# Kernel optimization log

Hardware: AMD Instinct MI355X
Metric: run time of the kernel (lower is better)

## Reference

```python
import jax, jax.numpy as jnp
import numpy as np

B, H, W = 2, 56, 56
D_MODEL, D_STATE, D_CONV, DT_RANK, K = 96, 16, 3, 6, 4
D_INNER = 192  # expand=2.0 * d_model


def _hscan1(x):
    # torch get_horizontal_scan1: flip odd columns along H; involution. x: (B,C,H,W)
    cols = (jnp.arange(x.shape[3]) % 2) == 1
    return jnp.where(cols[None, None, None, :], x[:, :, ::-1, :], x)


def _vscan1(x):
    # torch get_vertical_scan1: flip odd rows along W, then transpose H<->W. (B,C,H,W)->(B,C,W,H)
    rows = (jnp.arange(x.shape[2]) % 2) == 1
    x = jnp.where(rows[None, None, :, None], x[:, :, :, ::-1], x)
    return jnp.swapaxes(x, 2, 3)


def _revert_vscan1(x):
    # inverse of _vscan1. x: (B,C,W,H) -> (B,C,H,W)
    x = jnp.swapaxes(x, 2, 3)
    rows = (jnp.arange(x.shape[2]) % 2) == 1
    return jnp.where(rows[None, None, :, None], x[:, :, :, ::-1], x)


def _selective_scan(u, delta, A, Bs, Cs, D, delta_bias):
    # u, delta: (B, K*d, L); A: (K*d, N); Bs, Cs: (B, K, N, L); D: (K*d,)
    Bb, KD, L = u.shape
    k = Bs.shape[1]
    d = KD // k
    N = A.shape[1]
    delta = jax.nn.softplus(delta + delta_bias[None, :, None])
    u4 = u.reshape(Bb, k, d, L)
    dt4 = delta.reshape(Bb, k, d, L)
    A4 = A.reshape(k, d, N)
    dA = jnp.exp(jnp.einsum('bkdl,kdn->lbkdn', dt4, A4))           # (L,B,K,d,N)
    dBu = jnp.einsum('bkdl,bknl,bkdl->lbkdn', dt4, Bs, u4)          # (L,B,K,d,N)
    Ct = jnp.transpose(Cs, (3, 0, 1, 2))                            # (L,B,K,N)
    h0 = jnp.zeros((Bb, k, d, N), u.dtype)

    def step(h, inp):
        dA_t, dBu_t, C_t = inp
        h = dA_t * h + dBu_t
        y = jnp.einsum('bkdn,bkn->bkd', h, C_t)
        return h, y

    _, ys = jax.lax.scan(step, h0, (dA, dBu, Ct))                   # ys: (L,B,K,d)
    y = jnp.transpose(ys, (1, 2, 3, 0)).reshape(Bb, KD, L)
    return y + u * D[None, :, None]


def reference(x, in_proj_w, conv_w, conv_b, x_proj_weight, dt_projs_weight,
              dt_projs_bias, A_logs, Ds, out_norm_w, out_norm_b, out_proj_w):
    Bb, Hh, Ww, _ = x.shape
    L = Hh * Ww
    xz = jnp.einsum('bhwc,ec->bhwe', x, in_proj_w)
    xc, z = jnp.split(xz, 2, axis=-1)
    xc = jnp.transpose(xc, (0, 3, 1, 2))                            # (B, d_inner, H, W)
    xc = jax.lax.conv_general_dilated(xc, conv_w, (1, 1), ((1, 1), (1, 1)),
                                      feature_group_count=D_INNER)
    xc = jax.nn.silu(xc + conv_b[None, :, None, None])
    # torch code mutates x in place: vertical scan sees the h-scanned tensor
    x1 = _hscan1(xc)
    x_hw = x1.reshape(Bb, 1, D_INNER, L)
    x2 = _vscan1(x1)
    x_wh = x2.reshape(Bb, 1, D_INNER, L)
    xs = jnp.concatenate([x_hw, x_wh, x_hw[..., ::-1], x_wh[..., ::-1]], axis=1)  # (B,K,d,L)
    x_dbl = jnp.einsum('bkdl,kcd->bkcl', xs, x_proj_weight)
    dts, Bs, Cs = jnp.split(x_dbl, [DT_RANK, DT_RANK + D_STATE], axis=2)
    dts = jnp.einsum('bkrl,kdr->bkdl', dts, dt_projs_weight)
    u = xs.reshape(Bb, K * D_INNER, L)
    delta = dts.reshape(Bb, K * D_INNER, L)
    A = -jnp.exp(A_logs)
    out_y = _selective_scan(u, delta, A, Bs, Cs, Ds, dt_projs_bias.reshape(-1))
    oy = out_y.reshape(Bb, K, D_INNER, L)
    # revert scans back to a common spatial layout and sum
    s0 = _hscan1(oy[:, 0].reshape(Bb, D_INNER, Hh, Ww))
    s2 = _hscan1(oy[:, 2, :, ::-1].reshape(Bb, D_INNER, Hh, Ww))
    s1 = _hscan1(_revert_vscan1(oy[:, 1].reshape(Bb, D_INNER, Ww, Hh)))
    s3 = _hscan1(_revert_vscan1(oy[:, 3, :, ::-1].reshape(Bb, D_INNER, Ww, Hh)))
    y = (s0 + s1 + s2 + s3).reshape(Bb, D_INNER, L)
    y = jnp.transpose(y, (0, 2, 1))                                 # (B, L, d_inner)
    mu = jnp.mean(y, axis=-1, keepdims=True)
    var = jnp.var(y, axis=-1, keepdims=True)
    y = (y - mu) / jnp.sqrt(var + 1e-5) * out_norm_w + out_norm_b
    y = y.reshape(Bb, Hh, Ww, D_INNER) * jax.nn.silu(z)
    return jnp.einsum('bhwd,cd->bhwc', y, out_proj_w)


def setup_inputs():
    key = jax.random.key(0)
    ks = jax.random.split(key, 8)
    s = 0.02
    return {
        "x": jax.random.normal(ks[0], (B, H, W, D_MODEL), jnp.float32),
        "in_proj_w": jax.random.normal(ks[1], (2 * D_INNER, D_MODEL), jnp.float32) * s,
        "conv_w": jax.random.normal(ks[2], (D_INNER, 1, D_CONV, D_CONV), jnp.float32) * s,
        "conv_b": jnp.zeros((D_INNER,), jnp.float32),
        "x_proj_weight": jax.random.normal(ks[3], (K, DT_RANK + 2 * D_STATE, D_INNER), jnp.float32) * s,
        "dt_projs_weight": jax.random.normal(ks[4], (K, D_INNER, DT_RANK), jnp.float32) * (DT_RANK ** -0.5),
        "dt_projs_bias": jax.random.uniform(ks[5], (K, D_INNER), jnp.float32, -4.6, -2.3),
        "A_logs": jnp.log(jnp.tile(jnp.arange(1, D_STATE + 1, dtype=jnp.float32)[None, :], (K * D_INNER, 1))),
        "Ds": jnp.ones((K * D_INNER,), jnp.float32),
        "out_norm_w": jnp.ones((D_INNER,), jnp.float32),
        "out_norm_b": jnp.zeros((D_INNER,), jnp.float32),
        "out_proj_w": jax.random.normal(ks[6], (D_MODEL, D_INNER), jnp.float32) * s,
    }
```

## Files before the change

kernel.cpp:

```cpp
#include <hip/hip_runtime.h>
#include <hip/hip_bf16.h>

#define BB 2
#define HH 56
#define WW 56
#define LL (HH*WW)
#define DM 96
#define DI 192
#define NS 16
#define DTR 6
#define KK 4
#define CDBL (DTR + 2*NS)
#define CS 32
#define NC 98
#define ROWS (BB*KK*DI)

#define IP_BM 32
__global__ __launch_bounds__(256) void k_inproj(const float* __restrict__ x,
                                                const float* __restrict__ w,
                                                float* __restrict__ xcpre,
                                                float* __restrict__ zsilu) {
    __shared__ float xl[IP_BM*100];
    __shared__ float wl[64*100];
    int t = threadIdx.x;
    int bl0 = blockIdx.x * IP_BM;
    for (int idx = t; idx < IP_BM*96; idx += 256) {
        int r = idx/96, c = idx%96;
        xl[r*100+c] = x[(bl0+r)*DM + c];
    }
    int pg = t >> 4, eg = t & 15;
    for (int nc = 0; nc < 6; ++nc) {
        __syncthreads();
        for (int idx = t; idx < 64*96; idx += 256) {
            int r = idx/96, c = idx%96;
            wl[r*100+c] = w[(nc*64+r)*DM + c];
        }
        __syncthreads();
        float acc[2][4] = {};
        #pragma unroll 4
        for (int k = 0; k < 96; ++k) {
            float a0 = xl[(pg*2+0)*100+k];
            float a1 = xl[(pg*2+1)*100+k];
            float b0 = wl[(eg*4+0)*100+k];
            float b1 = wl[(eg*4+1)*100+k];
            float b2 = wl[(eg*4+2)*100+k];
            float b3 = wl[(eg*4+3)*100+k];
            acc[0][0] = fmaf(a0,b0,acc[0][0]); acc[0][1] = fmaf(a0,b1,acc[0][1]);
            acc[0][2] = fmaf(a0,b2,acc[0][2]); acc[0][3] = fmaf(a0,b3,acc[0][3]);
            acc[1][0] = fmaf(a1,b0,acc[1][0]); acc[1][1] = fmaf(a1,b1,acc[1][1]);
            acc[1][2] = fmaf(a1,b2,acc[1][2]); acc[1][3] = fmaf(a1,b3,acc[1][3]);
        }
        #pragma unroll
        for (int j = 0; j < 2; ++j) {
            int bl = bl0 + pg*2 + j;
            #pragma unroll
            for (int jj = 0; jj < 4; ++jj) {
                int e = nc*64 + eg*4 + jj;
                float v = acc[j][jj];
                if (e < DI) xcpre[(size_t)bl*DI + e] = v;
                else        zsilu[(size_t)bl*DI + (e-DI)] = v / (1.f + expf(-v));
            }
        }
    }
}

__global__ __launch_bounds__(DI) void k_conv(const float* __restrict__ xcpre,
                                             const float* __restrict__ cw,
                                             const float* __restrict__ cb,
                                             float* __restrict__ xs0,
                                             float* __restrict__ xs1) {
    int bl = blockIdx.x;
    int b = bl / LL, l = bl % LL;
    int h = l / WW, w = l % WW;
    int c = threadIdx.x;
    float acc = cb[c];
    #pragma unroll
    for (int dh = -1; dh <= 1; ++dh) {
        int hh = h + dh;
        if (hh < 0 || hh >= HH) continue;
        #pragma unroll
        for (int dw = -1; dw <= 1; ++dw) {
            int ww2 = w + dw;
            if (ww2 < 0 || ww2 >= WW) continue;
            acc = fmaf(xcpre[(b*LL + hh*WW + ww2)*DI + c],
                       cw[c*9 + (dh+1)*3 + (dw+1)], acc);
        }
    }
    float v = acc / (1.f + expf(-acc));
    int i  = (w & 1) ? (HH-1-h) : h;
    int l0 = i*WW + w;
    int l1 = ((i & 1) ? (WW-1-w) : w)*HH + i;
    xs0[(b*LL + l0)*DI + c] = v;
    xs1[(b*LL + l1)*DI + c] = v;
}

#define TL 32
__global__ __launch_bounds__(256) void k_proj(const float* __restrict__ xs0,
                                              const float* __restrict__ xs1,
                                              const float* __restrict__ xpw,
                                              const float* __restrict__ dtw,
                                              const float* __restrict__ dtb,
                                              float* __restrict__ delta,
                                              float* __restrict__ Bsb,
                                              float* __restrict__ Csb) {
    int tile = blockIdx.x, k = blockIdx.y, b = blockIdx.z;
    int t = threadIdx.x;
    __shared__ float Wl[CDBL*DI];
    __shared__ float dtWl[DI*DTR];
    __shared__ float dtbl[DI];
    __shared__ float Xl[TL*193];
    __shared__ float dblL[DTR*33];

    for (int idx = t; idx < CDBL*DI; idx += 256) Wl[idx] = xpw[k*CDBL*DI + idx];
    for (int idx = t; idx < DI*DTR;  idx += 256) dtWl[idx] = dtw[k*DI*DTR + idx];
    if (t < DI) dtbl[t] = dtb[k*DI + t];
    const float* src = (k & 1) ? xs1 : xs0;
    for (int idx = t; idx < TL*DI; idx += 256) {
        int ll = idx / DI, i = idx % DI;
        int lg = tile*TL + ll;
        int lp = (k >= 2) ? (LL-1-lg) : lg;
        Xl[ll*193 + i] = src[(b*LL + lp)*DI + i];
    }
    __syncthreads();

    for (int idx = t; idx < CDBL*TL; idx += 256) {
        int c = idx >> 5, ll = idx & 31;
        float acc = 0.f;
        #pragma unroll 8
        for (int i = 0; i < DI; ++i) acc = fmaf(Wl[c*DI + i], Xl[ll*193 + i], acc);
        int lg = tile*TL + ll;
        if (c < DTR) {
            dblL[c*33 + ll] = acc;
        } else if (c < DTR + NS) {
            Bsb[((b*KK + k)*LL + lg)*NS + (c - DTR)] = acc;
        } else {
            Csb[((b*KK + k)*LL + lg)*NS + (c - DTR - NS)] = acc;
        }
    }
    __syncthreads();

    for (int idx = t; idx < DI*TL; idx += 256) {
        int d = idx % DI, ll = idx / DI;
        float acc = dtbl[d];
        #pragma unroll
        for (int r = 0; r < DTR; ++r) acc = fmaf(dtWl[d*DTR + r], dblL[r*33 + ll], acc);
        float sp = fmaxf(acc, 0.f) + log1pf(expf(-fabsf(acc)));
        delta[((b*KK + k)*LL + tile*TL + ll)*DI + d] = sp;
    }
}

__global__ __launch_bounds__(192) void k_scan1(const float* __restrict__ delta,
                                               const float* __restrict__ xs0,
                                               const float* __restrict__ xs1,
                                               const float* __restrict__ Bsb,
                                               const float* __restrict__ A_logs,
                                               float* __restrict__ P,
                                               float* __restrict__ Hend) {
    int c = blockIdx.x, bk = blockIdx.y;
    int k = bk & 3, b = bk >> 2;
    int d = threadIdx.x;
    int kd = k*DI + d;
    __shared__ float Bl[CS*NS];
    const float* bsrc = Bsb + ((size_t)bk*LL + c*CS)*NS;
    for (int i = threadIdx.x; i < CS*NS/4; i += 192)
        ((float4*)Bl)[i] = ((const float4*)bsrc)[i];

    float A[NS], h[NS], p[NS];
    #pragma unroll
    for (int q = 0; q < 4; ++q) {
        float4 av = *(const float4*)&A_logs[kd*NS + 4*q];
        A[4*q+0] = -expf(av.x); A[4*q+1] = -expf(av.y);
        A[4*q+2] = -expf(av.z); A[4*q+3] = -expf(av.w);
    }
    #pragma unroll
    for (int n = 0; n < NS; ++n) { h[n] = 0.f; p[n] = 1.f; }
    __syncthreads();

    const bool rev = (k >= 2);
    const float* dp = delta + ((size_t)bk*LL + c*CS)*DI + d;
    const float* up = ((k & 1) ? xs1 : xs0) + (size_t)b*LL*DI + d;
    const int l0 = c*CS;

    #pragma unroll 2
    for (int i = 0; i < CS; ++i) {
        float dt = dp[(size_t)i*DI];
        int lp = rev ? (LL-1-(l0+i)) : (l0+i);
        float u = up[(size_t)lp*DI];
        float dtu = dt * u;
        float Bv[NS];
        #pragma unroll
        for (int q = 0; q < 4; ++q)
            *(float4*)&Bv[4*q] = *(const float4*)&Bl[i*NS + 4*q];
        #pragma unroll
        for (int n = 0; n < NS; ++n) {
            float dA = __expf(dt * A[n]);
            h[n] = fmaf(dA, h[n], dtu * Bv[n]);
            p[n] *= dA;
        }
    }
    size_t obase = ((size_t)c*ROWS + bk*DI + d)*NS;
    #pragma unroll
    for (int q = 0; q < 4; ++q) {
        *(float4*)&P[obase + 4*q]    = make_float4(p[4*q], p[4*q+1], p[4*q+2], p[4*q+3]);
        *(float4*)&Hend[obase + 4*q] = make_float4(h[4*q], h[4*q+1], h[4*q+2], h[4*q+3]);
    }
}

__global__ __launch_bounds__(256) void k_scanmid(const float* __restrict__ P,
                                                 const float* __restrict__ Hend,
                                                 float* __restrict__ Hin) {
    int tid = blockIdx.x*256 + threadIdx.x;
    float h = 0.f;
    for (int c = 0; c < NC; ++c) {
        size_t idx = (size_t)c*(ROWS*NS) + tid;
        Hin[idx] = h;
        h = fmaf(P[idx], h, Hend[idx]);
    }
}

__global__ __launch_bounds__(192) void k_scan2(const float* __restrict__ delta,
                                               const float* __restrict__ xs0,
                                               const float* __restrict__ xs1,
                                               const float* __restrict__ Bsb,
                                               const float* __restrict__ Csb,
                                               const float* __restrict__ A_logs,
                                               const float* __restrict__ Ds,
                                               const float* __restrict__ Hin,
                                               float* __restrict__ oy) {
    int c = blockIdx.x, bk = blockIdx.y;
    int k = bk & 3, b = bk >> 2;
    int d = threadIdx.x;
    int kd = k*DI + d;
    __shared__ float Bl[CS*NS];
    __shared__ float Cl[CS*NS];
    const float* bsrc = Bsb + ((size_t)bk*LL + c*CS)*NS;
    const float* csrc = Csb + ((size_t)bk*LL + c*CS)*NS;
    for (int i = threadIdx.x; i < CS*NS/4; i += 192) {
        ((float4*)Bl)[i] = ((const float4*)bsrc)[i];
        ((float4*)Cl)[i] = ((const float4*)csrc)[i];
    }

    float A[NS], h[NS];
    #pragma unroll
    for (int q = 0; q < 4; ++q) {
        float4 av = *(const float4*)&A_logs[kd*NS + 4*q];
        A[4*q+0] = -expf(av.x); A[4*q+1] = -expf(av.y);
        A[4*q+2] = -expf(av.z); A[4*q+3] = -expf(av.w);
    }
    size_t ibase = ((size_t)c*ROWS + bk*DI + d)*NS;
    #pragma unroll
    for (int q = 0; q < 4; ++q) {
        float4 hv = *(const float4*)&Hin[ibase + 4*q];
        h[4*q+0] = hv.x; h[4*q+1] = hv.y; h[4*q+2] = hv.z; h[4*q+3] = hv.w;
    }
    const float Dv = Ds[kd];
    __syncthreads();

    const bool rev = (k >= 2);
    const float* dp = delta + ((size_t)bk*LL + c*CS)*DI + d;
    const float* up = ((k & 1) ? xs1 : xs0) + (size_t)b*LL*DI + d;
    float* yp = oy + ((size_t)bk*LL + c*CS)*DI + d;
    const int l0 = c*CS;

    #pragma unroll 2
    for (int i = 0; i < CS; ++i) {
        float dt = dp[(size_t)i*DI];
        int lp = rev ? (LL-1-(l0+i)) : (l0+i);
        float u = up[(size_t)lp*DI];
        float dtu = dt * u;
        float Bv[NS], Cv[NS];
        #pragma unroll
        for (int q = 0; q < 4; ++q) {
            *(float4*)&Bv[4*q] = *(const float4*)&Bl[i*NS + 4*q];
            *(float4*)&Cv[4*q] = *(const float4*)&Cl[i*NS + 4*q];
        }
        float acc = 0.f;
        #pragma unroll
        for (int n = 0; n < NS; ++n) {
            float dA = __expf(dt * A[n]);
            h[n] = fmaf(dA, h[n], dtu * Bv[n]);
            acc = fmaf(h[n], Cv[n], acc);
        }
        yp[(size_t)i*DI] = fmaf(u, Dv, acc);
    }
}

#define OP_BM 32
__global__ __launch_bounds__(256) void k_out(const float* __restrict__ oy,
                                             const float* __restrict__ zsilu,
                                             const float* __restrict__ onw,
                                             const float* __restrict__ onb,
                                             const float* __restrict__ opw,
                                             float* __restrict__ out) {
    __shared__ float yv[OP_BM*196];
    __shared__ float wl[96*68];
    int t = threadIdx.x;
    int bl0 = blockIdx.x * OP_BM;
    int lane = t & 63, wv = t >> 6;

    for (int pp = 0; pp < 8; ++pp) {
        int p = wv*8 + pp;
        int bl = bl0 + p;
        int b = bl / LL, l = bl % LL;
        int h = l / WW, w2 = l % WW;
        int i = (w2 & 1) ? (HH-1-h) : h;
        int l0 = i*WW + w2;
        int l1 = ((i & 1) ? (WW-1-w2) : w2)*HH + i;
        size_t base = (size_t)b*KK*LL*DI;
        float yd[3]; float s1 = 0.f, s2 = 0.f;
        #pragma unroll
        for (int j = 0; j < 3; ++j) {
            int c = lane + j*64;
            float v = oy[base + (size_t)(0*LL + l0)*DI + c]
                    + oy[base + (size_t)(1*LL + l1)*DI + c]
                    + oy[base + (size_t)(2*LL + (LL-1-l0))*DI + c]
                    + oy[base + (size_t)(3*LL + (LL-1-l1))*DI + c];
            yd[j] = v; s1 += v; s2 += v*v;
        }
        #pragma unroll
        for (int m = 1; m < 64; m <<= 1) { s1 += __shfl_xor(s1, m); s2 += __shfl_xor(s2, m); }
        float mu  = s1 / DI;
        float var = s2 / DI - mu*mu;
        float ry  = rsqrtf(var + 1e-5f);
        #pragma unroll
        for (int j = 0; j < 3; ++j) {
            int c = lane + j*64;
            float yn = (yd[j] - mu) * ry * onw[c] + onb[c];
            yv[p*196 + c] = yn * zsilu[(size_t)bl*DI + c];
        }
    }

    int pg = t >> 5, eg = t & 31;
    float acc[4][3] = {};
    for (int kc = 0; kc < 3; ++kc) {
        __syncthreads();
        for (int idx = t; idx < 96*64; idx += 256) {
            int r = idx >> 6, c = idx & 63;
            wl[r*68 + c] = opw[r*DI + kc*64 + c];
        }
        __syncthreads();
        #pragma unroll 4
        for (int kk = 0; kk < 64; ++kk) {
            float a[4], bq[3];
            #pragma unroll
            for (int j = 0; j < 4; ++j)  a[j]  = yv[(pg*4+j)*196 + kc*64 + kk];
            #pragma unroll
            for (int jj = 0; jj < 3; ++jj) bq[jj] = wl[(eg*3+jj)*68 + kk];
            #pragma unroll
            for (int j = 0; j < 4; ++j)
                #pragma unroll
                for (int jj = 0; jj < 3; ++jj)
                    acc[j][jj] = fmaf(a[j], bq[jj], acc[j][jj]);
        }
    }
    #pragma unroll
    for (int j = 0; j < 4; ++j) {
        int bl = bl0 + pg*4 + j;
        #pragma unroll
        for (int jj = 0; jj < 3; ++jj)
            out[(size_t)bl*DM + eg*3 + jj] = acc[j][jj];
    }
}

extern "C" void kernel_launch(void* const* d_in, const int* in_sizes, int n_in,
                              void* d_out, int out_size, void* d_ws, size_t ws_size,
                              hipStream_t stream) {
    const float* x      = (const float*)d_in[0];
    const float* ipw    = (const float*)d_in[1];
    const float* convw  = (const float*)d_in[2];
    const float* convb  = (const float*)d_in[3];
    const float* xpw    = (const float*)d_in[4];
    const float* dtw    = (const float*)d_in[5];
    const float* dtb    = (const float*)d_in[6];
    const float* A_logs = (const float*)d_in[7];
    const float* Ds     = (const float*)d_in[8];
    const float* onw    = (const float*)d_in[9];
    const float* onb    = (const float*)d_in[10];
    const float* opw    = (const float*)d_in[11];
    float* out = (float*)d_out;

    float* ws = (float*)d_ws;
    const size_t SZ_BLD  = (size_t)BB*LL*DI;
    const size_t SZ_BKLD = (size_t)BB*KK*LL*DI;
    const size_t SZ_BKLN = (size_t)BB*KK*LL*NS;
    const size_t SZ_ST   = (size_t)NC*ROWS*NS;
    float* xcpre = ws;
    float* zsilu = xcpre + SZ_BLD;
    float* xs0   = zsilu + SZ_BLD;
    float* xs1   = xs0   + SZ_BLD;
    float* delta = xs1   + SZ_BLD;
    float* Bsb   = delta + SZ_BKLD;
    float* Csb   = Bsb   + SZ_BKLN;
    float* oy    = Csb   + SZ_BKLN;
    float* Hin   = oy    + SZ_BKLD;
    float* Hend  = oy;
    float* P     = oy + SZ_ST;

    k_inproj<<<(BB*LL)/IP_BM, 256, 0, stream>>>(x, ipw, xcpre, zsilu);
    k_conv<<<BB*LL, DI, 0, stream>>>(xcpre, convw, convb, xs0, xs1);
    dim3 g3(LL/TL, KK, BB);
    k_proj<<<g3, 256, 0, stream>>>(xs0, xs1, xpw, dtw, dtb, delta, Bsb, Csb);
    dim3 gs(NC, BB*KK);
    k_scan1<<<gs, 192, 0, stream>>>(delta, xs0, xs1, Bsb, A_logs, P, Hend);
    k_scanmid<<<(ROWS*NS)/256, 256, 0, stream>>>(P, Hend, Hin);
    k_scan2<<<gs, 192, 0, stream>>>(delta, xs0, xs1, Bsb, Csb, A_logs, Ds, Hin, oy);
    k_out<<<(BB*LL)/OP_BM, 256, 0, stream>>>(oy, zsilu, onw, onb, opw, out);
}
```

Before: 273.7 us.

## Register-block x_proj GEMM in k_proj with K-chunked shared tiles

Rewrites k_proj so the x_proj matmul streams K in 48-wide chunks through small shared tiles with float4 loads. Each thread computes a 3x4 register block of outputs over a 64-position tile. The tile was 32 positions and one dot product per thread. dt_proj weights and biases now sit in registers, exploiting that each thread's channel index is fixed across iterations. The aim is less shared memory, higher occupancy and more FMA reuse per load, at the cost of extra syncs and half as many blocks.

```diff
diff --git a/kernel.cpp b/kernel.cpp
--- a/kernel.cpp
+++ b/kernel.cpp
@@ -94,7 +94,11 @@
     xs1[(b*LL + l1)*DI + c] = v;
 }
 
-#define TL 32
+#define TL 64
+#define KCH 48
+#define NKC 4
+#define XSTR 52
+#define WSTR 52
 __global__ __launch_bounds__(256) void k_proj(const float* __restrict__ xs0,
                                               const float* __restrict__ xs1,
                                               const float* __restrict__ xpw,
@@ -104,48 +108,118 @@
                                               float* __restrict__ Bsb,
                                               float* __restrict__ Csb) {
     int tile = blockIdx.x, k = blockIdx.y, b = blockIdx.z;
+    int bk = b*KK + k;
     int t = threadIdx.x;
-    __shared__ float Wl[CDBL*DI];
-    __shared__ float dtWl[DI*DTR];
-    __shared__ float dtbl[DI];
-    __shared__ float Xl[TL*193];
-    __shared__ float dblL[DTR*33];
-
-    for (int idx = t; idx < CDBL*DI; idx += 256) Wl[idx] = xpw[k*CDBL*DI + idx];
-    for (int idx = t; idx < DI*DTR;  idx += 256) dtWl[idx] = dtw[k*DI*DTR + idx];
-    if (t < DI) dtbl[t] = dtb[k*DI + t];
+    __shared__ float Xl[TL*XSTR];
+    __shared__ float Wl[39*WSTR];
+    __shared__ float dblL[DTR*68];
+
     const float* src = (k & 1) ? xs1 : xs0;
-    for (int idx = t; idx < TL*DI; idx += 256) {
-        int ll = idx / DI, i = idx % DI;
-        int lg = tile*TL + ll;
-        int lp = (k >= 2) ? (LL-1-lg) : lg;
-        Xl[ll*193 + i] = src[(b*LL + lp)*DI + i];
+    const bool rev = (k >= 2);
+    int cp = t >> 4, lp = t & 15;
+
+    float acc[3][4] = {};
+    for (int kc = 0; kc < NKC; ++kc) {
+        __syncthreads();
+        for (int idx = t; idx < 39*12; idx += 256) {
+            int r = idx/12, q = idx%12;
+            float4 v = (r < CDBL)
+                ? ((const float4*)(xpw + (size_t)k*CDBL*DI + (size_t)r*DI + kc*KCH))[q]
+                : make_float4(0.f,0.f,0.f,0.f);
+            *(float4*)&Wl[r*WSTR + 4*q] = v;
+        }
+        for (int idx = t; idx < TL*12; idx += 256) {
+            int ll = idx/12, q = idx%12;
+            int lg = tile*TL + ll;
+            int lpos = rev ? (LL-1-lg) : lg;
+            *(float4*)&Xl[ll*XSTR + 4*q] =
+                ((const float4*)(src + (size_t)(b*LL + lpos)*DI + kc*KCH))[q];
+        }
+        __syncthreads();
+        if (cp < 13) {
+            const float4* w0 = (const float4*)&Wl[(3*cp+0)*WSTR];
+            const float4* w1 = (const float4*)&Wl[(3*cp+1)*WSTR];
+            const float4* w2 = (const float4*)&Wl[(3*cp+2)*WSTR];
+            const float4* x0 = (const float4*)&Xl[(lp    )*XSTR];
+            const float4* x1 = (const float4*)&Xl[(lp+16)*XSTR];
+            const float4* x2 = (const float4*)&Xl[(lp+32)*XSTR];
+            const float4* x3 = (const float4*)&Xl[(lp+48)*XSTR];
+            #pragma unroll
+            for (int q = 0; q < 12; ++q) {
+                float4 wa = w0[q], wb = w1[q], wc = w2[q];
+                float4 xa = x0[q], xb = x1[q], xc = x2[q], xd = x3[q];
+                acc[0][0]=fmaf(wa.x,xa.x,acc[0][0]); acc[0][0]=fmaf(wa.y,xa.y,acc[0][0]);
+                acc[0][0]=fmaf(wa.z,xa.z,acc[0][0]); acc[0][0]=fmaf(wa.w,xa.w,acc[0][0]);
+                acc[0][1]=fmaf(wa.x,xb.x,acc[0][1]); acc[0][1]=fmaf(wa.y,xb.y,acc[0][1]);
+                acc[0][1]=fmaf(wa.z,xb.z,acc[0][1]); acc[0][1]=fmaf(wa.w,xb.w,acc[0][1]);
+                acc[0][2]=fmaf(wa.x,xc.x,acc[0][2]); acc[0][2]=fmaf(wa.y,xc.y,acc[0][2]);
+                acc[0][2]=fmaf(wa.z,xc.z,acc[0][2]); acc[0][2]=fmaf(wa.w,xc.w,acc[0][2]);
+                acc[0][3]=fmaf(wa.x,xd.x,acc[0][3]); acc[0][3]=fmaf(wa.y,xd.y,acc[0][3]);
+                acc[0][3]=fmaf(wa.z,xd.z,acc[0][3]); acc[0][3]=fmaf(wa.w,xd.w,acc[0][3]);
+                acc[1][0]=fmaf(wb.x,xa.x,acc[1][0]); acc[1][0]=fmaf(wb.y,xa.y,acc[1][0]);
+                acc[1][0]=fmaf(wb.z,xa.z,acc[1][0]); acc[1][0]=fmaf(wb.w,xa.w,acc[1][0]);
+                acc[1][1]=fmaf(wb.x,xb.x,acc[1][1]); acc[1][1]=fmaf(wb.y,xb.y,acc[1][1]);
+                acc[1][1]=fmaf(wb.z,xb.z,acc[1][1]); acc[1][1]=fmaf(wb.w,xb.w,acc[1][1]);
+                acc[1][2]=fmaf(wb.x,xc.x,acc[1][2]); acc[1][2]=fmaf(wb.y,xc.y,acc[1][2]);
+                acc[1][2]=fmaf(wb.z,xc.z,acc[1][2]); acc[1][2]=fmaf(wb.w,xc.w,acc[1][2]);
+                acc[1][3]=fmaf(wb.x,xd.x,acc[1][3]); acc[1][3]=fmaf(wb.y,xd.y,acc[1][3]);
+                acc[1][3]=fmaf(wb.z,xd.z,acc[1][3]); acc[1][3]=fmaf(wb.w,xd.w,acc[1][3]);
+                acc[2][0]=fmaf(wc.x,xa.x,acc[2][0]); acc[2][0]=fmaf(wc.y,xa.y,acc[2][0]);
+                acc[2][0]=fmaf(wc.z,xa.z,acc[2][0]); acc[2][0]=fmaf(wc.w,xa.w,acc[2][0]);
+                acc[2][1]=fmaf(wc.x,xb.x,acc[2][1]); acc[2][1]=fmaf(wc.y,xb.y,acc[2][1]);
+                acc[2][1]=fmaf(wc.z,xb.z,acc[2][1]); acc[2][1]=fmaf(wc.w,xb.w,acc[2][1]);
+                acc[2][2]=fmaf(wc.x,xc.x,acc[2][2]); acc[2][2]=fmaf(wc.y,xc.y,acc[2][2]);
+                acc[2][2]=fmaf(wc.z,xc.z,acc[2][2]); acc[2][2]=fmaf(wc.w,xc.w,acc[2][2]);
+                acc[2][3]=fmaf(wc.x,xd.x,acc[2][3]); acc[2][3]=fmaf(wc.y,xd.y,acc[2][3]);
+                acc[2][3]=fmaf(wc.z,xd.z,acc[2][3]); acc[2][3]=fmaf(wc.w,xd.w,acc[2][3]);
+            }
+        }
+    }
+    if (cp < 13) {
+        #pragma unroll
+        for (int ci = 0; ci < 3; ++ci) {
+            int c = 3*cp + ci;
+            if (c < CDBL) {
+                #pragma unroll
+                for (int li = 0; li < 4; ++li) {
+                    int ll = lp + 16*li;
+                    int lg = tile*TL + ll;
+                    float v = acc[ci][li];
+                    if (c < DTR)          dblL[c*68 + ll] = v;
+                    else if (c < DTR+NS)  Bsb[((size_t)bk*LL + lg)*NS + (c-DTR)] = v;
+                    else                  Csb[((size_t)bk*LL + lg)*NS + (c-DTR-NS)] = v;
+                }
+            }
+        }
     }
     __syncthreads();
 
-    for (int idx = t; idx < CDBL*TL; idx += 256) {
-        int c = idx >> 5, ll = idx & 31;
-        float acc = 0.f;
-        #pragma unroll 8
-        for (int i = 0; i < DI; ++i) acc = fmaf(Wl[c*DI + i], Xl[ll*193 + i], acc);
-        int lg = tile*TL + ll;
-        if (c < DTR) {
-            dblL[c*33 + ll] = acc;
-        } else if (c < DTR + NS) {
-            Bsb[((b*KK + k)*LL + lg)*NS + (c - DTR)] = acc;
-        } else {
-            Csb[((b*KK + k)*LL + lg)*NS + (c - DTR - NS)] = acc;
-        }
-    }
-    __syncthreads();
-
-    for (int idx = t; idx < DI*TL; idx += 256) {
-        int d = idx % DI, ll = idx / DI;
-        float acc = dtbl[d];
-        #pragma unroll
-        for (int r = 0; r < DTR; ++r) acc = fmaf(dtWl[d*DTR + r], dblL[r*33 + ll], acc);
-        float sp = fmaxf(acc, 0.f) + log1pf(expf(-fabsf(acc)));
-        delta[((b*KK + k)*LL + tile*TL + ll)*DI + d] = sp;
+    float wr0[DTR], wr1[DTR], wr2[DTR], bb0, bb1, bb2;
+    {
+        int d0 = t % DI, d1 = (t+64) % DI, d2 = (t+128) % DI;
+        #pragma unroll
+        for (int r = 0; r < DTR; ++r) {
+            wr0[r] = dtw[((size_t)k*DI + d0)*DTR + r];
+            wr1[r] = dtw[((size_t)k*DI + d1)*DTR + r];
+            wr2[r] = dtw[((size_t)k*DI + d2)*DTR + r];
+        }
+        bb0 = dtb[k*DI + d0]; bb1 = dtb[k*DI + d1]; bb2 = dtb[k*DI + d2];
+    }
+    float* dbase = delta + ((size_t)bk*LL + (size_t)tile*TL)*DI;
+    for (int j3 = 0; j3 < 16; ++j3) {
+        #pragma unroll
+        for (int jj = 0; jj < 3; ++jj) {
+            int j = j3*3 + jj;
+            int idx = t + 256*j;
+            int d = idx % DI;
+            int ll = idx / DI;
+            float a = (jj == 0) ? bb0 : (jj == 1) ? bb1 : bb2;
+            const float* wrp = (jj == 0) ? wr0 : (jj == 1) ? wr1 : wr2;
+            #pragma unroll
+            for (int r = 0; r < DTR; ++r) a = fmaf(wrp[r], dblL[r*68 + ll], a);
+            float sp = fmaxf(a, 0.f) + log1pf(expf(-fabsf(a)));
+            dbase[(size_t)ll*DI + d] = sp;
+        }
     }
 }
 
```

Result: faster. 259.0 us (-5.4%).
